# Optimization experiments

Measured on AMD Instinct MI355X. Metric: run time of the kernel, lower is better.

## Reference

```python
import jax, jax.numpy as jnp
import numpy as np

H, FF = 4096, 14336   # hidden size, SwiGLU intermediate size
B, S = 4, 2048        # batch, sequence length


def setup_inputs() -> dict:
    key = jax.random.key(0)
    ks = jax.random.split(key, 7)
    x = jax.random.normal(ks[0], (B, S, H), dtype=jnp.float32)
    # Ternary weights: values in {-1, 0, +1}
    gate_t = jax.random.randint(ks[1], (FF, H), -1, 2, dtype=jnp.int32)
    up_t = jax.random.randint(ks[2], (FF, H), -1, 2, dtype=jnp.int32)
    down_t = jax.random.randint(ks[3], (H, FF), -1, 2, dtype=jnp.int32)
    # Per-output-row scales (positive, realistic quantization scale magnitudes)
    gate_s = jax.random.uniform(ks[4], (FF,), jnp.float32, 0.01, 0.1)
    up_s = jax.random.uniform(ks[5], (FF,), jnp.float32, 0.01, 0.1)
    down_s = jax.random.uniform(ks[6], (H,), jnp.float32, 0.01, 0.1)
    return {"x": x, "gate_t": gate_t, "up_t": up_t, "down_t": down_t,
            "gate_s": gate_s, "up_s": up_s, "down_s": down_s}


def reference(x, gate_t, up_t, down_t, gate_s, up_s, down_s):
    # SwiGLU forward with on-the-fly ternary dequant, matching
    # TernaryExpertModule.forward (output_proj=None).
    Bb, Ss, Hh = x.shape
    x_flat = x.reshape(Bb * Ss, Hh)                         # [BS, H]
    gate_w = gate_t.astype(jnp.float32) * gate_s[:, None]   # [FF, H]
    up_w = up_t.astype(jnp.float32) * up_s[:, None]         # [FF, H]
    down_w = down_t.astype(jnp.float32) * down_s[:, None]   # [H, FF]
    gate_out = x_flat @ gate_w.T                            # [BS, FF]
    up_out = x_flat @ up_w.T                                # [BS, FF]
    hidden = jax.nn.silu(gate_out) * up_out                 # [BS, FF]
    out_flat = hidden @ down_w.T                            # [BS, H]
    return out_flat.reshape(Bb, Ss, -1)
```

## Files before the change

kernel.cpp:

```cpp
#include <hip/hip_runtime.h>
#include <stdint.h>

#define H_DIM   4096
#define FF_DIM  14336
#define M_TOK   8192
#define KC1     (H_DIM / 32)
#define KC2     (FF_DIM / 32)
#define NC1     (H_DIM / 64)
#define CPX     (H_DIM / 32)

typedef unsigned short ushort_t;
typedef __attribute__((ext_vector_type(8)))  short bf16x8;
typedef __attribute__((ext_vector_type(4)))  float f32x4;
typedef __attribute__((ext_vector_type(4)))  int   i32x4;
typedef __attribute__((ext_vector_type(16))) int   i32x16;

__device__ __forceinline__ unsigned short f2bf(float f) {
    union { float f; uint32_t u; } v; v.f = f;
    uint32_t r = v.u + 0x7FFFu + ((v.u >> 16) & 1u);
    return (unsigned short)(r >> 16);
}
__device__ __forceinline__ unsigned short t2bf(int v) {
    unsigned int mag = (v & 1) ? 0x3F80u : 0u;
    unsigned int sgn = ((unsigned int)v >> 16) & 0x8000u;
    return (unsigned short)(mag | sgn);
}
__device__ __forceinline__ bf16x8 pack_f8(f32x4 a, f32x4 b) {
    bf16x8 o;
    o[0]=(short)f2bf(a[0]); o[1]=(short)f2bf(a[1]); o[2]=(short)f2bf(a[2]); o[3]=(short)f2bf(a[3]);
    o[4]=(short)f2bf(b[0]); o[5]=(short)f2bf(b[1]); o[6]=(short)f2bf(b[2]); o[7]=(short)f2bf(b[3]);
    return o;
}
__device__ __forceinline__ bf16x8 pack_t8(i32x4 a, i32x4 b) {
    bf16x8 o;
    o[0]=(short)t2bf(a[0]); o[1]=(short)t2bf(a[1]); o[2]=(short)t2bf(a[2]); o[3]=(short)t2bf(a[3]);
    o[4]=(short)t2bf(b[0]); o[5]=(short)t2bf(b[1]); o[6]=(short)t2bf(b[2]); o[7]=(short)t2bf(b[3]);
    return o;
}
__device__ __forceinline__ int pack4(int a, int b, int c, int d) {
    return (a & 255) | ((b & 255) << 8) | ((c & 255) << 16) | ((d & 255) << 24);
}

#define GLDS16(gp, lp) __builtin_amdgcn_global_load_lds( \
    (__attribute__((address_space(1))) void*)(gp),       \
    (__attribute__((address_space(3))) void*)(lp), 16, 0, 0)

#define WAITVM8 asm volatile("s_waitcnt vmcnt(8)" ::: "memory")
#define WAITVM4 asm volatile("s_waitcnt vmcnt(4)" ::: "memory")
#define WAITVM0 asm volatile("s_waitcnt vmcnt(0)" ::: "memory")
#define SBAR    asm volatile("s_barrier" ::: "memory")


template<int K, bool TERN>
__global__ __launch_bounds__(256)
void k_cvt_lds(const void* __restrict__ inv, unsigned short* __restrict__ out) {
    constexpr int KC = K / 32;
    constexpr int CP = K / 64;
    __shared__ int sm[128][68];
    const int b   = blockIdx.x;
    const int t   = b / CP;
    const int cp  = b % CP;
    const int tid = threadIdx.x;
    const int rr  = tid >> 4;
    const int c4  = (tid & 15) * 4;
    const int k0  = cp * 64;

    const int* in = (const int*)inv;
    #pragma unroll
    for (int p = 0; p < 8; ++p) {
        const int row = p * 16 + rr;
        *(i32x4*)&sm[row][c4] = *(const i32x4*)(in + (size_t)(t * 128 + row) * K + k0 + c4);
    }
    __syncthreads();
    #pragma unroll
    for (int p = 0; p < 4; ++p) {
        const int idx = p * 256 + tid;
        const int cc  = idx >> 9;
        const int f   = (idx >> 6) & 7;
        const int l   = idx & 63;
        const int row = f * 16 + (l & 15);
        const int kl  = cc * 32 + (l >> 4) * 8;
        bf16x8 o;
        if (TERN) {
            i32x4 a = *(const i32x4*)&sm[row][kl];
            i32x4 bq = *(const i32x4*)&sm[row][kl + 4];
            o = pack_t8(a, bq);
        } else {
            f32x4 a = *(const f32x4*)&sm[row][kl];
            f32x4 bq = *(const f32x4*)&sm[row][kl + 4];
            o = pack_f8(a, bq);
        }
        *(bf16x8*)(out + (((size_t)t * KC + (cp * 2 + cc)) * 8 + f) * 512 + (size_t)l * 8) = o;
    }
}

__global__ __launch_bounds__(256)
void k_amax(const float* __restrict__ x, float* __restrict__ sx, float* __restrict__ rsx) {
    const int row  = blockIdx.x * 4 + (threadIdx.x >> 6);
    const int lane = threadIdx.x & 63;
    const f32x4* p = (const f32x4*)(x + (size_t)row * H_DIM);
    float m = 0.f;
    #pragma unroll 4
    for (int i = lane; i < H_DIM / 4; i += 64) {
        f32x4 v = p[i];
        m = fmaxf(m, fmaxf(fmaxf(fabsf(v[0]), fabsf(v[1])), fmaxf(fabsf(v[2]), fabsf(v[3]))));
    }
    #pragma unroll
    for (int o = 32; o; o >>= 1) m = fmaxf(m, __shfl_xor(m, o, 64));
    if (lane == 0) {
        sx[row]  = m * (1.f / 127.f);
        rsx[row] = m > 0.f ? 127.f / m : 0.f;
    }
}

template<int K, bool TERN>
__global__ __launch_bounds__(256)
void k_cvt_i8(const void* __restrict__ inv, const float* __restrict__ rsx,
              char* __restrict__ out) {
    constexpr int CP = K / 32;
    __shared__ int sm[128][68];
    const int b   = blockIdx.x;
    const int t   = b / (K / 64);
    const int cp  = b % (K / 64);
    const int tid = threadIdx.x;
    const int rr  = tid >> 4;
    const int c4  = (tid & 15) * 4;

    const int* in = (const int*)inv;
    #pragma unroll
    for (int p = 0; p < 8; ++p) {
        const int row = p * 16 + rr;
        *(i32x4*)&sm[row][c4] = *(const i32x4*)(in + (size_t)(t * 128 + row) * K + cp * 64 + c4);
    }
    __syncthreads();
    #pragma unroll
    for (int p = 0; p < 2; ++p) {
        const int pos = p * 256 + tid;
        const int cc  = pos >> 8;
        const int f   = (pos >> 6) & 3;
        const int l   = pos & 63;
        const int row = f * 32 + (l & 31);
        const int kb  = cc * 32 + (l >> 5) * 16;
        i32x4 o;
        if constexpr (TERN) {
            #pragma unroll
            for (int q = 0; q < 4; ++q)
                o[q] = pack4(sm[row][kb + q * 4], sm[row][kb + q * 4 + 1],
                             sm[row][kb + q * 4 + 2], sm[row][kb + q * 4 + 3]);
        } else {
            const float rs = rsx[t * 128 + row];
            #pragma unroll
            for (int q = 0; q < 4; ++q) {
                const float* fp = (const float*)&sm[row][kb + q * 4];
                o[q] = pack4(__float2int_rn(fp[0] * rs), __float2int_rn(fp[1] * rs),
                             __float2int_rn(fp[2] * rs), __float2int_rn(fp[3] * rs));
            }
        }
        *(i32x4*)(out + ((size_t)(t * CP + cp * 2 + cc) * 4 + f) * 1024 + (size_t)l * 16) = o;
    }
}

__global__ __launch_bounds__(512, 2)
void k_gemm1_i8(const char* __restrict__ xq,
                const char* __restrict__ gq, const char* __restrict__ uq,
                const float* __restrict__ sxp,
                const float* __restrict__ gs, const float* __restrict__ us,
                ushort_t* __restrict__ hid)
{
    __shared__ char lds[131072];
    const int tid  = threadIdx.x;
    const int lane = tid & 63;
    const int wv   = tid >> 6;
    const int wr   = wv >> 1;
    const int wc   = wv & 1;
    const int l31  = lane & 31;
    const int lhi  = lane >> 5;

    const int bid = blockIdx.x;
    const int bmt = bid & 31;
    const int bnt = bid >> 5;

    const char* xa0  = xq + (size_t)(2 * bmt)     * CPX * 4096;
    const char* xa1  = xq + (size_t)(2 * bmt + 1) * CPX * 4096;
    const char* srcA = (tid < 256 ? xa0 : xa1 - 4096) + tid * 16;
    const char* gbb  = gq + (size_t)bnt * CPX * 4096;
    const char* ubb  = uq + (size_t)bnt * CPX * 4096;

    i32x16 accg[2][2] = {};
    i32x16 accu[2][2] = {};
    i32x4  af[2][2], afn[2][2];

#define STAGE1(h) { char* sl_ = lds + ((h) & 3) * 32768;                     \
    GLDS16(srcA + (size_t)(h) * 8192,           sl_ + tid * 16);             \
    GLDS16(srcA + (size_t)(h) * 8192 + 4096,    sl_ + 8192  + tid * 16);     \
    GLDS16(gbb  + (size_t)(h) * 8192 + tid * 16, sl_ + 16384 + tid * 16);    \
    GLDS16(ubb  + (size_t)(h) * 8192 + tid * 16, sl_ + 24576 + tid * 16); }

    STAGE1(0); STAGE1(1); STAGE1(2);
    WAITVM8;
    SBAR;
    #pragma unroll
    for (int c2 = 0; c2 < 2; ++c2)
        #pragma unroll
        for (int i = 0; i < 2; ++i)
            af[c2][i] = *(const i32x4*)(lds + c2 * 8192 + (wr * 2 + i) * 1024 + lane * 16);

#define G1BODY(WAITOP, DO_STAGE, DO_AFN)                                            \
  {                                                                                 \
    char* slot = lds + (H & 3) * 32768;                                             \
    WAITOP;                                              \
    SBAR;               \
    if (DO_STAGE) STAGE1(H + 3);                                                    \
    i32x4 gf[2][2], uf[2][2];                                                       \
    _Pragma("unroll")                                                               \
    for (int c2 = 0; c2 < 2; ++c2)                                                  \
      _Pragma("unroll")                                                             \
      for (int n = 0; n < 2; ++n) {                                                 \
        gf[c2][n] = *(const i32x4*)(slot + 16384 + c2 * 4096 + (wc * 2 + n) * 1024 + lane * 16); \
        uf[c2][n] = *(const i32x4*)(slot + 24576 + c2 * 4096 + (wc * 2 + n) * 1024 + lane * 16); \
      }                                                                             \
    if (DO_AFN) {                                                                   \
      char* sn = lds + ((H + 1) & 3) * 32768;                                       \
      _Pragma("unroll")                                                             \
      for (int c2 = 0; c2 < 2; ++c2)                                                \
        _Pragma("unroll")                                                           \
        for (int i = 0; i < 2; ++i)                                                 \
          afn[c2][i] = *(const i32x4*)(sn + c2 * 8192 + (wr * 2 + i) * 1024 + lane * 16); \
    }                                                                               \
    __builtin_amdgcn_s_setprio(1);                                                  \
    _Pragma("unroll")                                                               \
    for (int c2 = 0; c2 < 2; ++c2)                                                  \
      _Pragma("unroll")                                                             \
      for (int i = 0; i < 2; ++i)                                                   \
        _Pragma("unroll")                                                           \
        for (int n = 0; n < 2; ++n)                                                 \
          accg[i][n] = __builtin_amdgcn_mfma_i32_32x32x32_i8(af[c2][i], gf[c2][n], accg[i][n], 0, 0, 0); \
    _Pragma("unroll")                                                               \
    for (int c2 = 0; c2 < 2; ++c2)                                                  \
      _Pragma("unroll")                                                             \
      for (int i = 0; i < 2; ++i)                                                   \
        _Pragma("unroll")                                                           \
        for (int n = 0; n < 2; ++n)                                                 \
          accu[i][n] = __builtin_amdgcn_mfma_i32_32x32x32_i8(af[c2][i], uf[c2][n], accu[i][n], 0, 0, 0); \
    __builtin_amdgcn_s_setprio(0);                                                  \
    if (DO_AFN) {                                                                   \
      _Pragma("unroll")                                                             \
      for (int c2 = 0; c2 < 2; ++c2)                                                \
        _Pragma("unroll")                                                           \
        for (int i = 0; i < 2; ++i) af[c2][i] = afn[c2][i];                         \
    }                                                                               \
  }

    int H = 0;
    for (; H < NC1 - 3; ++H) G1BODY(WAITVM4, 1, 1);
    G1BODY(WAITVM4, 0, 1); ++H;
    G1BODY(WAITVM0, 0, 1); ++H;
    G1BODY(WAITVM0, 0, 0);
#undef G1BODY
#undef STAGE1

    const int bm0 = bmt * 256;
    const int bn0 = bnt * 128;
    #pragma unroll
    for (int i = 0; i < 2; ++i) {
        #pragma unroll
        for (int n = 0; n < 2; ++n) {
            const int col = bn0 + wc * 64 + n * 32 + l31;
            const float sg = gs[col];
            const float su = us[col];
            const int c  = col >> 5;
            const int lp = ((col & 31) >> 3) * 16;
            const int e  = col & 7;
            #pragma unroll
            for (int reg = 0; reg < 16; ++reg) {
                const int row32 = (reg & 3) + 8 * (reg >> 2) + 4 * lhi;
                const int row = bm0 + wr * 64 + i * 32 + row32;
                const float sx = sxp[row];
                float g = (float)accg[i][n][reg] * (sx * sg);
                float u = (float)accu[i][n][reg] * (sx * su);
                float hv = g * (1.0f / (1.0f + __expf(-g))) * u;
                const int t = row >> 7;
                const int f = (row >> 4) & 7;
                const int l = (row & 15) + lp;
                hid[(((size_t)t * KC2 + c) * 8 + f) * 512 + l * 8 + e] = f2bf(hv);
            }
        }
    }
}

__global__ __launch_bounds__(512, 2)
void k_gemm2_8p(const ushort_t* __restrict__ hid, const ushort_t* __restrict__ db,
                const float* __restrict__ dsc, float* __restrict__ out)
{
    __shared__ ushort_t lds[65536];
    const int tid  = threadIdx.x;
    const int lane = tid & 63;
    const int wv   = tid >> 6;
    const int wr   = wv >> 2;
    const int wc   = wv & 3;
    const int l15  = lane & 15;
    const int lq   = lane >> 4;

    const int bid = blockIdx.x;
    const int bmt = bid & 31;
    const int bnt = bid >> 5;

    const ushort_t* ha0 = hid + ((size_t)(bmt * 2)     * KC2) * 4096;
    const ushort_t* ha1 = hid + ((size_t)(bmt * 2 + 1) * KC2) * 4096;
    const ushort_t* db0 = db  + ((size_t)(bnt * 2)     * KC2) * 4096;
    const ushort_t* db1 = db  + ((size_t)(bnt * 2 + 1) * KC2) * 4096;

    f32x4 acc[8][4] = {};

    #pragma unroll
    for (int h = 0; h < 3; ++h) {
        ushort_t* sl = lds + h * 16384;
        GLDS16(ha0 + (size_t)h * 4096 + tid * 8, sl + tid * 8);
        GLDS16(ha1 + (size_t)h * 4096 + tid * 8, sl + 4096 + tid * 8);
        GLDS16(db0 + (size_t)h * 4096 + tid * 8, sl + 8192 + tid * 8);
        GLDS16(db1 + (size_t)h * 4096 + tid * 8, sl + 12288 + tid * 8);
    }

#define G2_HALF(WAITOP, DO_ISSUE)                                                  \
  {                                                                                \
    ushort_t* slot = lds + (H & 3) * 16384;                                        \
    const ushort_t* Ab = slot + wr * 4096 + lane * 8;                              \
    const ushort_t* Bb = slot + 8192 + (wc >> 1) * 4096 + ((wc & 1) * 4) * 512 + lane * 8; \
    WAITOP;                                                                        \
    SBAR;                                                                          \
    bf16x8 af[4], bfv[4];                                                          \
    _Pragma("unroll")                                                              \
    for (int m = 0; m < 4; m++) af[m] = *(const bf16x8*)(Ab + m * 512);            \
    _Pragma("unroll")                                                              \
    for (int n = 0; n < 4; n++) bfv[n] = *(const bf16x8*)(Bb + n * 512);           \
    if (DO_ISSUE) {                                                                \
      const int Hp = H + 3;                                                        \
      ushort_t* sp = lds + (Hp & 3) * 16384;                                       \
      GLDS16(ha0 + (size_t)Hp * 4096 + tid * 8, sp + tid * 8);                     \
      GLDS16(ha1 + (size_t)Hp * 4096 + tid * 8, sp + 4096 + tid * 8);              \
    }                                                                              \
    __builtin_amdgcn_s_setprio(1);                                                 \
    _Pragma("unroll")                                                              \
    for (int m = 0; m < 4; m++)                                                    \
      _Pragma("unroll")                                                            \
      for (int n = 0; n < 4; n++)                                                  \
        acc[m][n] = __builtin_amdgcn_mfma_f32_16x16x32_bf16(af[m], bfv[n], acc[m][n], 0, 0, 0); \
    __builtin_amdgcn_s_setprio(0);                                                 \
    SBAR;                                                                          \
    bf16x8 af2[4];                                                                 \
    _Pragma("unroll")                                                              \
    for (int m = 0; m < 4; m++) af2[m] = *(const bf16x8*)(Ab + (4 + m) * 512);     \
    if (DO_ISSUE) {                                                                \
      const int Hp = H + 3;                                                        \
      ushort_t* sp = lds + (Hp & 3) * 16384;                                       \
      GLDS16(db0 + (size_t)Hp * 4096 + tid * 8, sp + 8192 + tid * 8);              \
      GLDS16(db1 + (size_t)Hp * 4096 + tid * 8, sp + 12288 + tid * 8);             \
    }                                                                              \
    __builtin_amdgcn_s_setprio(1);                                                 \
    _Pragma("unroll")                                                              \
    for (int m = 0; m < 4; m++)                                                    \
      _Pragma("unroll")                                                            \
      for (int n = 0; n < 4; n++)                                                  \
        acc[4 + m][n] = __builtin_amdgcn_mfma_f32_16x16x32_bf16(af2[m], bfv[n], acc[4 + m][n], 0, 0, 0); \
    __builtin_amdgcn_s_setprio(0);                                                 \
  }

    int H = 0;
    for (; H < KC2 - 3; ++H) G2_HALF(WAITVM8, 1);
    G2_HALF(WAITVM8, 0); ++H;
    G2_HALF(WAITVM4, 0); ++H;
    G2_HALF(WAITVM0, 0);
#undef G2_HALF

    const int bm0 = bmt * 256;
    const int bn0 = bnt * 256;
    #pragma unroll
    for (int n = 0; n < 4; n++) {
        const int gcol = bn0 + wc * 64 + n * 16 + l15;
        const float sd = dsc[gcol];
        #pragma unroll
        for (int m = 0; m < 8; m++) {
            const int grow = bm0 + wr * 128 + m * 16 + lq * 4;
            #pragma unroll
            for (int r = 0; r < 4; r++)
                out[(size_t)(grow + r) * H_DIM + gcol] = acc[m][n][r] * sd;
        }
    }
}

__device__ __forceinline__ void ds_write_frag(ushort_t* buf, int crow, int ccol,
                                              bf16x8 lo, bf16x8 hi) {
    int f  = crow >> 4;
    int la = (crow & 15) + (((ccol)     & 31) >> 3) * 16;
    int lb = (crow & 15) + (((ccol + 8) & 31) >> 3) * 16;
    *(bf16x8*)&buf[f * 512 + la * 8] = lo;
    *(bf16x8*)&buf[f * 512 + lb * 8] = hi;
}

template<bool PREA>
__global__ __launch_bounds__(256, 2)
void k_gemm1_fb(const float* __restrict__ xf, const ushort_t* __restrict__ xb,
                const int* __restrict__ gt, const int* __restrict__ ut,
                const float* __restrict__ gs, const float* __restrict__ us,
                ushort_t* __restrict__ hid)
{
    __shared__ ushort_t As[4096];
    __shared__ ushort_t Gs[4096];
    __shared__ ushort_t Us[4096];

    const int tid  = threadIdx.x;
    const int lane = tid & 63;
    const int wv   = tid >> 6;
    const int wr   = wv >> 1;
    const int wc   = wv & 1;
    const int l15  = lane & 15;
    const int lq   = lane >> 4;

    const int bid = blockIdx.x;
    const int bmt = bid & 63;
    const int bnt = bid >> 6;
    const int bm0 = bmt * 128;
    const int bn0 = bnt * 128;

    f32x4 accg[4][4] = {};
    f32x4 accu[4][4] = {};

    const ushort_t* pa = PREA ? xb + (size_t)bmt * KC1 * 4096 : nullptr;
    const int crow = tid >> 1;
    const int ccol = (tid & 1) * 16;

    for (int kc = 0; kc < KC1; kc++) {
        __syncthreads();
        const int k0 = kc * 32;
        if constexpr (PREA) {
            GLDS16(pa + tid * 8,        &As[tid * 8]);
            GLDS16(pa + tid * 8 + 2048, &As[tid * 8 + 2048]);
        } else {
            const float* xa = xf + (size_t)(bm0 + crow) * H_DIM + k0 + ccol;
            f32x4 a0 = ((const f32x4*)xa)[0], a1 = ((const f32x4*)xa)[1];
            f32x4 a2 = ((const f32x4*)xa)[2], a3 = ((const f32x4*)xa)[3];
            ds_write_frag(As, crow, ccol, pack_f8(a0, a1), pack_f8(a2, a3));
        }
        {
            const size_t wo = (size_t)(bn0 + crow) * H_DIM + k0 + ccol;
            const i32x4* gp = (const i32x4*)(gt + wo);
            i32x4 g0 = gp[0], g1 = gp[1], g2 = gp[2], g3 = gp[3];
            ds_write_frag(Gs, crow, ccol, pack_t8(g0, g1), pack_t8(g2, g3));
            const i32x4* up = (const i32x4*)(ut + wo);
            i32x4 u0 = up[0], u1 = up[1], u2 = up[2], u3 = up[3];
            ds_write_frag(Us, crow, ccol, pack_t8(u0, u1), pack_t8(u2, u3));
        }
        __syncthreads();

        bf16x8 af[4], gf[4], uf[4];
        #pragma unroll
        for (int m = 0; m < 4; m++)
            af[m] = *(const bf16x8*)&As[(wr * 4 + m) * 512 + lane * 8];
        #pragma unroll
        for (int n = 0; n < 4; n++) {
            gf[n] = *(const bf16x8*)&Gs[(wc * 4 + n) * 512 + lane * 8];
            uf[n] = *(const bf16x8*)&Us[(wc * 4 + n) * 512 + lane * 8];
        }
        #pragma unroll
        for (int m = 0; m < 4; m++)
            #pragma unroll
            for (int n = 0; n < 4; n++) {
                accg[m][n] = __builtin_amdgcn_mfma_f32_16x16x32_bf16(af[m], gf[n], accg[m][n], 0, 0, 0);
                accu[m][n] = __builtin_amdgcn_mfma_f32_16x16x32_bf16(af[m], uf[n], accu[m][n], 0, 0, 0);
            }
        if constexpr (PREA) pa += 4096;
    }

    #pragma unroll
    for (int n = 0; n < 4; n++) {
        const int gcol = bn0 + wc * 64 + n * 16 + l15;
        const float sg = gs[gcol];
        const float su = us[gcol];
        const int c  = gcol >> 5;
        const int lp = ((gcol & 31) >> 3) * 16;
        const int e  = gcol & 7;
        #pragma unroll
        for (int m = 0; m < 4; m++) {
            const int rb = bm0 + wr * 64 + m * 16 + lq * 4;
            #pragma unroll
            for (int r = 0; r < 4; r++) {
                const int row = rb + r;
                float g = accg[m][n][r] * sg;
                float u = accu[m][n][r] * su;
                float hv = g * (1.0f / (1.0f + __expf(-g))) * u;
                const int t = row >> 7;
                const int f = (row >> 4) & 7;
                const int l = (row & 15) + lp;
                hid[(((size_t)t * KC2 + c) * 8 + f) * 512 + l * 8 + e] = f2bf(hv);
            }
        }
    }
}

__global__ __launch_bounds__(256, 2)
void k_gemm2_fb(const ushort_t* __restrict__ hid, const int* __restrict__ dt,
                const float* __restrict__ dsc, float* __restrict__ out)
{
    __shared__ ushort_t As[4096];
    __shared__ ushort_t Bs[4096];

    const int tid  = threadIdx.x;
    const int lane = tid & 63;
    const int wv   = tid >> 6;
    const int wr   = wv >> 1;
    const int wc   = wv & 1;
    const int l15  = lane & 15;
    const int lq   = lane >> 4;

    const int bid = blockIdx.x;
    const int bmt = bid & 63;
    const int bnt = bid >> 6;
    const int bm0 = bmt * 128;
    const int bn0 = bnt * 128;

    f32x4 acc[4][4] = {};
    const ushort_t* pa = hid + (size_t)bmt * KC2 * 4096;
    const int crow = tid >> 1;
    const int ccol = (tid & 1) * 16;

    for (int kc = 0; kc < KC2; kc++) {
        __syncthreads();
        GLDS16(pa + tid * 8,        &As[tid * 8]);
        GLDS16(pa + tid * 8 + 2048, &As[tid * 8 + 2048]);
        {
            const i32x4* dp = (const i32x4*)(dt + (size_t)(bn0 + crow) * FF_DIM + kc * 32 + ccol);
            i32x4 d0 = dp[0], d1 = dp[1], d2 = dp[2], d3 = dp[3];
            ds_write_frag(Bs, crow, ccol, pack_t8(d0, d1), pack_t8(d2, d3));
        }
        __syncthreads();

        bf16x8 af[4], bfr[4];
        #pragma unroll
        for (int m = 0; m < 4; m++)
            af[m] = *(const bf16x8*)&As[(wr * 4 + m) * 512 + lane * 8];
        #pragma unroll
        for (int n = 0; n < 4; n++)
            bfr[n] = *(const bf16x8*)&Bs[(wc * 4 + n) * 512 + lane * 8];
        #pragma unroll
        for (int m = 0; m < 4; m++)
            #pragma unroll
            for (int n = 0; n < 4; n++)
                acc[m][n] = __builtin_amdgcn_mfma_f32_16x16x32_bf16(af[m], bfr[n], acc[m][n], 0, 0, 0);
        pa += 4096;
    }

    #pragma unroll
    for (int n = 0; n < 4; n++) {
        const int gcol = bn0 + wc * 64 + n * 16 + l15;
        const float sd = dsc[gcol];
        #pragma unroll
        for (int m = 0; m < 4; m++) {
            const int grow = bm0 + wr * 64 + m * 16 + lq * 4;
            #pragma unroll
            for (int r = 0; r < 4; r++)
                out[(size_t)(grow + r) * H_DIM + gcol] = acc[m][n][r] * sd;
        }
    }
}

extern "C" void kernel_launch(void* const* d_in, const int* in_sizes, int n_in,
                              void* d_out, int out_size, void* d_ws, size_t ws_size,
                              hipStream_t stream) {
    const float* xf  = (const float*)d_in[0];
    const int*   gt  = (const int*)d_in[1];
    const int*   ut  = (const int*)d_in[2];
    const int*   dt  = (const int*)d_in[3];
    const float* gsc = (const float*)d_in[4];
    const float* usc = (const float*)d_in[5];
    const float* dsc = (const float*)d_in[6];
    float* out = (float*)d_out;

    const size_t HID_B = (size_t)M_TOK * FF_DIM * 2;
    const size_t DB_B  = (size_t)FF_DIM * H_DIM * 2;
    const size_t G8_B  = (size_t)FF_DIM * H_DIM;
    const size_t U8_B  = (size_t)FF_DIM * H_DIM;
    const size_t X8_B  = (size_t)M_TOK * H_DIM;
    const size_t SX_B  = (size_t)M_TOK * 4;
    const size_t XB_B  = (size_t)M_TOK * H_DIM * 2;

    char* base = (char*)d_ws;
    ushort_t* hid = (ushort_t*)base;
    ushort_t* dbp = (ushort_t*)(base + HID_B);
    char*     g8  = base + HID_B + DB_B;
    char*     u8  = g8 + G8_B;
    char*     x8  = u8 + U8_B;
    float*    sxp = (float*)(x8 + X8_B);
    float*    rsx = sxp + M_TOK;
    ushort_t* xbp = (ushort_t*)(base + HID_B);

    const bool has_w  = ws_size >= HID_B + DB_B + G8_B + U8_B + X8_B + 2 * SX_B;
    const bool has_xb = ws_size >= HID_B + XB_B;

    if (has_w) {
        k_amax<<<M_TOK / 4, 256, 0, stream>>>(xf, sxp, rsx);
        k_cvt_i8<H_DIM,  false><<<(M_TOK / 128) * (H_DIM / 64), 256, 0, stream>>>(xf, rsx, x8);
        k_cvt_i8<H_DIM,  true ><<<(FF_DIM / 128) * (H_DIM / 64), 256, 0, stream>>>(gt, nullptr, g8);
        k_cvt_i8<H_DIM,  true ><<<(FF_DIM / 128) * (H_DIM / 64), 256, 0, stream>>>(ut, nullptr, u8);
        k_cvt_lds<FF_DIM, true><<<(H_DIM / 128) * (FF_DIM / 64), 256, 0, stream>>>(dt, dbp);

        k_gemm1_i8<<<32 * 112, 512, 0, stream>>>(x8, g8, u8, sxp, gsc, usc, hid);
        k_gemm2_8p<<<32 * 16, 512, 0, stream>>>(hid, dbp, dsc, out);
    } else {
        const int grid1 = 64 * 112;
        const int grid2 = 64 * 32;
        if (has_xb) {
            k_cvt_lds<H_DIM, false><<<(M_TOK / 128) * (H_DIM / 64), 256, 0, stream>>>(xf, xbp);
            k_gemm1_fb<true><<<grid1, 256, 0, stream>>>(nullptr, xbp, gt, ut, gsc, usc, hid);
        } else {
            k_gemm1_fb<false><<<grid1, 256, 0, stream>>>(xf, nullptr, gt, ut, gsc, usc, hid);
        }
        k_gemm2_fb<<<grid2, 256, 0, stream>>>(hid, dt, dsc, out);
    }
}
```

Before: 1.814 ms.

## Load GEMM1 activation fragments directly to registers and double-buffer weight fragments

The first int8 GEMM (gate/up projection) no longer stages activation tiles through shared memory. Each wave now loads its A fragments straight from global memory into a double-buffered register set two steps ahead, and only the gate/up weight tiles go through LDS. Weight fragments are read from LDS one stage ahead into ping-pong registers, so MFMA work overlaps the next stage's loads. The LDS footprint is halved, which could allow a second resident block per CU, but the two waves sharing a row band now fetch the same A data redundantly from cache, and register pressure rises.

Measured after the change: 1.955 ms. 1.08x slower.

```diff
diff --git a/kernel.cpp b/kernel.cpp
--- a/kernel.cpp
+++ b/kernel.cpp
@@ -45,10 +45,12 @@
     (__attribute__((address_space(1))) void*)(gp),       \
     (__attribute__((address_space(3))) void*)(lp), 16, 0, 0)
 
-#define WAITVM8 asm volatile("s_waitcnt vmcnt(8)" ::: "memory")
-#define WAITVM4 asm volatile("s_waitcnt vmcnt(4)" ::: "memory")
-#define WAITVM0 asm volatile("s_waitcnt vmcnt(0)" ::: "memory")
-#define SBAR    asm volatile("s_barrier" ::: "memory")
+#define WAITVM12 asm volatile("s_waitcnt vmcnt(12)" ::: "memory")
+#define WAITVM10 asm volatile("s_waitcnt vmcnt(10)" ::: "memory")
+#define WAITVM8  asm volatile("s_waitcnt vmcnt(8)" ::: "memory")
+#define WAITVM4  asm volatile("s_waitcnt vmcnt(4)" ::: "memory")
+#define WAITVM0  asm volatile("s_waitcnt vmcnt(0)" ::: "memory")
+#define SBAR     asm volatile("s_barrier" ::: "memory")
 
 
 template<int K, bool TERN>
@@ -167,7 +169,7 @@
                 const float* __restrict__ gs, const float* __restrict__ us,
                 ushort_t* __restrict__ hid)
 {
-    __shared__ char lds[131072];
+    __shared__ char lds[65536];
     const int tid  = threadIdx.x;
     const int lane = tid & 63;
     const int wv   = tid >> 6;
@@ -180,84 +182,60 @@
     const int bmt = bid & 31;
     const int bnt = bid >> 5;
 
-    const char* xa0  = xq + (size_t)(2 * bmt)     * CPX * 4096;
-    const char* xa1  = xq + (size_t)(2 * bmt + 1) * CPX * 4096;
-    const char* srcA = (tid < 256 ? xa0 : xa1 - 4096) + tid * 16;
-    const char* gbb  = gq + (size_t)bnt * CPX * 4096;
-    const char* ubb  = uq + (size_t)bnt * CPX * 4096;
+    const char* gbb = gq + (size_t)bnt * CPX * 4096;
+    const char* ubb = uq + (size_t)bnt * CPX * 4096;
+    const char* aW  = xq + ((size_t)(2 * bmt + (wr >> 1)) * CPX) * 4096
+                         + ((wr & 1) * 2) * 1024 + lane * 16;
 
     i32x16 accg[2][2] = {};
     i32x16 accu[2][2] = {};
-    i32x4  af[2][2], afn[2][2];
-
-#define STAGE1(h) { char* sl_ = lds + ((h) & 3) * 32768;                     \
-    GLDS16(srcA + (size_t)(h) * 8192,           sl_ + tid * 16);             \
-    GLDS16(srcA + (size_t)(h) * 8192 + 4096,    sl_ + 8192  + tid * 16);     \
-    GLDS16(gbb  + (size_t)(h) * 8192 + tid * 16, sl_ + 16384 + tid * 16);    \
-    GLDS16(ubb  + (size_t)(h) * 8192 + tid * 16, sl_ + 24576 + tid * 16); }
-
-    STAGE1(0); STAGE1(1); STAGE1(2);
-    WAITVM8;
+    i32x4  afb[2][2][2];
+    i32x4  gfb[2][2][2], ufb[2][2][2];
+
+#define STG(h) { char* sl_ = lds + ((h) & 3) * 16384;                          \
+    GLDS16(gbb + (size_t)(h) * 8192 + tid * 16, sl_ + tid * 16);               \
+    GLDS16(ubb + (size_t)(h) * 8192 + tid * 16, sl_ + 8192 + tid * 16); }
+
+#define ALOAD(P, h) {                                                          \
+    _Pragma("unroll") for (int c2 = 0; c2 < 2; ++c2)                           \
+    _Pragma("unroll") for (int i = 0; i < 2; ++i)                              \
+        afb[P][c2][i] = *(const i32x4*)(aW + (size_t)(2 * (h) + c2) * 4096 + i * 1024); }
+
+#define PF(Q, h) { const char* sn_ = lds + ((h) & 3) * 16384;                  \
+    _Pragma("unroll") for (int c2 = 0; c2 < 2; ++c2)                           \
+    _Pragma("unroll") for (int n = 0; n < 2; ++n) {                            \
+        gfb[Q][c2][n] = *(const i32x4*)(sn_ + c2 * 4096 + (wc * 2 + n) * 1024 + lane * 16); \
+        ufb[Q][c2][n] = *(const i32x4*)(sn_ + 8192 + c2 * 4096 + (wc * 2 + n) * 1024 + lane * 16); } }
+
+#define MM(P) { __builtin_amdgcn_s_setprio(1);                                 \
+    _Pragma("unroll") for (int c2 = 0; c2 < 2; ++c2)                           \
+    _Pragma("unroll") for (int i = 0; i < 2; ++i)                              \
+    _Pragma("unroll") for (int n = 0; n < 2; ++n)                              \
+        accg[i][n] = __builtin_amdgcn_mfma_i32_32x32x32_i8(afb[P][c2][i], gfb[P][c2][n], accg[i][n], 0, 0, 0); \
+    _Pragma("unroll") for (int c2 = 0; c2 < 2; ++c2)                           \
+    _Pragma("unroll") for (int i = 0; i < 2; ++i)                              \
+    _Pragma("unroll") for (int n = 0; n < 2; ++n)                              \
+        accu[i][n] = __builtin_amdgcn_mfma_i32_32x32x32_i8(afb[P][c2][i], ufb[P][c2][n], accu[i][n], 0, 0, 0); \
+    __builtin_amdgcn_s_setprio(0); }
+
+    STG(0); STG(1); STG(2);
+    ALOAD(0, 0); ALOAD(1, 1);
+    WAITVM12;
     SBAR;
-    #pragma unroll
-    for (int c2 = 0; c2 < 2; ++c2)
-        #pragma unroll
-        for (int i = 0; i < 2; ++i)
-            af[c2][i] = *(const i32x4*)(lds + c2 * 8192 + (wr * 2 + i) * 1024 + lane * 16);
-
-#define G1BODY(WAITOP, DO_STAGE, DO_AFN)                                            \
-  {                                                                                 \
-    char* slot = lds + (H & 3) * 32768;                                             \
-    WAITOP;                                              \
-    SBAR;               \
-    if (DO_STAGE) STAGE1(H + 3);                                                    \
-    i32x4 gf[2][2], uf[2][2];                                                       \
-    _Pragma("unroll")                                                               \
-    for (int c2 = 0; c2 < 2; ++c2)                                                  \
-      _Pragma("unroll")                                                             \
-      for (int n = 0; n < 2; ++n) {                                                 \
-        gf[c2][n] = *(const i32x4*)(slot + 16384 + c2 * 4096 + (wc * 2 + n) * 1024 + lane * 16); \
-        uf[c2][n] = *(const i32x4*)(slot + 24576 + c2 * 4096 + (wc * 2 + n) * 1024 + lane * 16); \
-      }                                                                             \
-    if (DO_AFN) {                                                                   \
-      char* sn = lds + ((H + 1) & 3) * 32768;                                       \
-      _Pragma("unroll")                                                             \
-      for (int c2 = 0; c2 < 2; ++c2)                                                \
-        _Pragma("unroll")                                                           \
-        for (int i = 0; i < 2; ++i)                                                 \
-          afn[c2][i] = *(const i32x4*)(sn + c2 * 8192 + (wr * 2 + i) * 1024 + lane * 16); \
-    }                                                                               \
-    __builtin_amdgcn_s_setprio(1);                                                  \
-    _Pragma("unroll")                                                               \
-    for (int c2 = 0; c2 < 2; ++c2)                                                  \
-      _Pragma("unroll")                                                             \
-      for (int i = 0; i < 2; ++i)                                                   \
-        _Pragma("unroll")                                                           \
-        for (int n = 0; n < 2; ++n)                                                 \
-          accg[i][n] = __builtin_amdgcn_mfma_i32_32x32x32_i8(af[c2][i], gf[c2][n], accg[i][n], 0, 0, 0); \
-    _Pragma("unroll")                                                               \
-    for (int c2 = 0; c2 < 2; ++c2)                                                  \
-      _Pragma("unroll")                                                             \
-      for (int i = 0; i < 2; ++i)                                                   \
-        _Pragma("unroll")                                                           \
-        for (int n = 0; n < 2; ++n)                                                 \
-          accu[i][n] = __builtin_amdgcn_mfma_i32_32x32x32_i8(af[c2][i], uf[c2][n], accu[i][n], 0, 0, 0); \
-    __builtin_amdgcn_s_setprio(0);                                                  \
-    if (DO_AFN) {                                                                   \
-      _Pragma("unroll")                                                             \
-      for (int c2 = 0; c2 < 2; ++c2)                                                \
-        _Pragma("unroll")                                                           \
-        for (int i = 0; i < 2; ++i) af[c2][i] = afn[c2][i];                         \
-    }                                                                               \
-  }
-
-    int H = 0;
-    for (; H < NC1 - 3; ++H) G1BODY(WAITVM4, 1, 1);
-    G1BODY(WAITVM4, 0, 1); ++H;
-    G1BODY(WAITVM0, 0, 1); ++H;
-    G1BODY(WAITVM0, 0, 0);
-#undef G1BODY
-#undef STAGE1
+    PF(0, 0);
+
+    for (int H = 0; H < NC1 - 4; H += 2) {
+        WAITVM10; SBAR; PF(1, H + 1); STG(H + 3); MM(0); ALOAD(0, H + 2);
+        WAITVM10; SBAR; PF(0, H + 2); STG(H + 4); MM(1); ALOAD(1, H + 3);
+    }
+    WAITVM10; SBAR; PF(1, 61); STG(63); MM(0); ALOAD(0, 62);
+    WAITVM10; SBAR; PF(0, 62);          MM(1); ALOAD(1, 63);
+    WAITVM8;  SBAR; PF(1, 63);          MM(0);
+    WAITVM0;  SBAR;                     MM(1);
+#undef STG
+#undef ALOAD
+#undef PF
+#undef MM
 
     const int bm0 = bmt * 256;
     const int bn0 = bnt * 128;
```
